# Performance work log

Measured on AMD Instinct MI355X. Metric: run time of the kernel, lower is better.

Reference implementation:

```python
import jax, jax.numpy as jnp
import numpy as np

DX = 0.1
DY = 0.1
W_B = 1000.0
W_PARALLEL = 1000.0
W_DIV = 100.0
EPS = 1e-10


def setup_inputs() -> dict:
    key = jax.random.key(0)
    k1, k2 = jax.random.split(key)
    outputs = jax.random.normal(k1, (2, 3, 256, 256, 64), dtype=jnp.float32)
    targets = jax.random.normal(k2, (2, 4, 256, 256, 64), dtype=jnp.float32)
    return {"outputs": outputs, "targets": targets}


def _corners(f):
    # 8 shifted views f[..., i:, j:, k:] (with 0 -> [0:-1], 1 -> [1:]) on dims 2,3,4
    s0, s1 = slice(0, -1), slice(1, None)
    return {(i, j, k): f[:, :, (s1 if i else s0), (s1 if j else s0), (s1 if k else s0)]
            for i in (0, 1) for j in (0, 1) for k in (0, 1)}


def _forward(outputs, targets):
    bx_p, by_p, bz_p = outputs[:, 0:1], outputs[:, 1:2], outputs[:, 2:3]
    bx_t, by_t, bz_t = targets[:, 0:1], targets[:, 1:2], targets[:, 2:3]

    loss_b = (jnp.mean((bx_p**2 + by_p**2 - bx_t**2 - by_t**2) ** 2 / (bx_t**2 + by_t**2 + EPS))
              + jnp.mean((bz_p - bz_t) ** 4 / (bz_t**2 + EPS)))
    loss_parallel = jnp.mean((bx_p * by_t - by_p * bx_t) ** 2
                             / (bx_t**2 + by_t**2 + bz_t**2 + EPS))

    bx = _corners(bx_p)
    by = _corners(by_p)
    bz = _corners(bz_p)
    z = _corners(targets[:, 3:4])

    num = (0.25 * (bx[1, 0, 0] + bx[1, 1, 0] + bx[1, 0, 1] + bx[1, 1, 1]) * DY * 0.5 * (z[1, 0, 1] - z[1, 0, 0] + z[1, 1, 1] - z[1, 1, 0])
           - 0.25 * (bx[0, 0, 0] + bx[0, 1, 0] + bx[0, 0, 1] + bx[0, 1, 1]) * DY * 0.5 * (z[0, 0, 1] - z[0, 0, 0] + z[0, 1, 1] - z[0, 1, 0])
           + 0.25 * (by[0, 1, 0] + by[1, 1, 0] + by[0, 1, 1] + by[1, 1, 1]) * DX * 0.5 * (z[0, 1, 1] - z[0, 1, 0] + z[1, 1, 1] - z[1, 1, 0])
           - 0.25 * (by[0, 0, 0] + by[1, 0, 0] + by[0, 0, 1] + by[1, 0, 1]) * DX * 0.5 * (z[0, 0, 1] - z[0, 0, 0] + z[1, 0, 1] - z[1, 0, 0])
           + 0.25 * (bz[0, 0, 1] + bz[0, 1, 1] + bz[1, 0, 1] + bz[1, 1, 1]) * DX * DY
           - 0.25 * (bz[0, 0, 0] + bz[0, 1, 0] + bz[1, 0, 0] + bz[1, 1, 0]) * DX * DY
           + (bx[0, 0, 1] + bx[1, 0, 1] + bx[1, 1, 1]) * DY * (z[0, 0, 1] - z[1, 0, 1]) / 6
           + (bx[0, 1, 1] + bx[1, 1, 1] + bx[1, 0, 1]) * DY * (z[0, 1, 1] - z[1, 1, 1]) / 6
           + (by[1, 0, 1] + by[1, 1, 1] + by[0, 1, 1]) * DX * (z[1, 0, 1] - z[1, 1, 1]) / 6
           + (by[0, 0, 1] + by[0, 1, 1] + by[1, 1, 1]) * DX * (z[0, 0, 1] - z[0, 1, 1]) / 6
           - (bx[0, 0, 0] + bx[1, 0, 0] + bx[1, 1, 0]) * DY * (z[0, 0, 0] - z[1, 0, 0]) / 6
           - (bx[0, 1, 0] + bx[1, 1, 0] + bx[1, 0, 0]) * DY * (z[0, 1, 0] - z[1, 1, 0]) / 6
           - (by[1, 0, 0] + by[1, 1, 0] + by[0, 1, 0]) * DX * (z[1, 0, 0] - z[1, 1, 0]) / 6
           - (by[0, 0, 0] + by[0, 1, 0] + by[1, 1, 0]) * DX * (z[0, 0, 0] - z[0, 1, 0]) / 6)

    bx_c = sum(bx[c] for c in sorted(bx)) * 0.125
    by_c = sum(by[c] for c in sorted(by)) * 0.125
    bz_c = sum(bz[c] for c in sorted(bz)) * 0.125
    den = bx_c**2 + by_c**2 + bz_c**2 + EPS

    loss_div = jnp.mean(num**2 / den) / DX**2 / DY**2

    return (W_B * loss_b + W_PARALLEL * loss_parallel, W_DIV * loss_div)


def reference(outputs, targets):
    return _forward(outputs, targets)
```

## Files before the change

kernel.cpp:

```cpp
#include <hip/hip_runtime.h>
#include <stdint.h>

constexpr int B = 2, X = 256, Y = 256, Z = 64;
constexpr int CO = X * Y * Z;
constexpr int YZ = Y * Z;
constexpr long long N_PTS   = (long long)B * X * Y * Z;
constexpr long long M_CELLS = (long long)B * (X-1) * (Y-1) * (Z-1);

constexpr int RPB = 16;
constexpr int TPB = 256;
constexpr int WPB = TPB / 64;
constexpr int BLOCKS = B * (Y / RPB) * X;

constexpr int SSTRIDE = 1152;

#define EPSc 1e-10f
#define SIXTH (1.0f / 6.0f)
#define RCPF(v) __builtin_amdgcn_rcpf(v)

typedef float fvec4 __attribute__((ext_vector_type(4)));

#define F4C(v, c) (((c) == 0) ? (v).x : ((c) == 1) ? (v).y : ((c) == 2) ? (v).z : (v).w)

typedef const __attribute__((address_space(1))) uint32_t* gptr_t;
typedef __attribute__((address_space(3))) uint32_t* lptr_t;

__global__ __launch_bounds__(TPB, 4) void loss_main(const float* __restrict__ outs,
                                                    const float* __restrict__ tgts,
                                                    double* __restrict__ partial) {
    __shared__ float sm[8 * SSTRIDE];

    const int lane = threadIdx.x & 63;
    const int wv   = threadIdx.x >> 6;
    const int blk  = blockIdx.x;

    const int b  = blk >> 12;
    const int r  = blk & 4095;
    const int sy = r >> 8;
    const int x  = r & 255;
    const int y0 = sy * RPB;
    const int xc1 = (x + 1 < X) ? (x + 1) : (X - 1);
    const bool xvalid = (x < X - 1);

    const float* ob = outs + (size_t)b * 3 * CO;
    const float* tb = tgts + (size_t)b * 4 * CO;

    const int row_l = wv * 4 + (lane >> 4);
    const int zi    = (lane & 15) << 2;
    const int y_own = y0 + row_l;
    const bool yvalid = (y_own < Y - 1);

    const float* tb0 = tb + (size_t)x * YZ + (size_t)y_own * Z + zi;
    const fvec4 tbx = __builtin_nontemporal_load((const fvec4*)(tb0 + 0 * CO));
    const fvec4 tby = __builtin_nontemporal_load((const fvec4*)(tb0 + 1 * CO));
    const fvec4 tbz = __builtin_nontemporal_load((const fvec4*)(tb0 + 2 * CO));

    const int y16 = (y0 + 16 < Y) ? (y0 + 16) : (Y - 1);
    #pragma unroll
    for (int j = 0; j < 2; ++j) {
        const int s   = wv * 2 + j;
        const int col = s >> 2;
        const int ch  = s & 3;
        const int xs  = col ? xc1 : x;
        const float* gbase = (ch < 3 ? ob + (size_t)ch * CO : tb + (size_t)3 * CO)
                           + (size_t)xs * YZ;
        const float* gsrc  = gbase + (size_t)y0 * Z;
        float* ldst = sm + s * SSTRIDE;
        #pragma unroll
        for (int k = 0; k < 4; ++k) {
            __builtin_amdgcn_global_load_lds((gptr_t)(gsrc + k * 256 + lane * 4),
                                             (lptr_t)(ldst + k * 256 + lane * 4),
                                             16, 0, 0);
        }
        const float* gsrc16 = gbase + (size_t)y16 * Z;
        __builtin_amdgcn_global_load_lds((gptr_t)(gsrc16 + lane),
                                         (lptr_t)(ldst + 16 * 64 + lane),
                                         4, 0, 0);
    }
    __syncthreads();

    #define SMF4(col, ch, row) (*(const fvec4*)(sm + ((col) * 4 + (ch)) * SSTRIDE + (row) * 64 + zi))

    const fvec4 obx   = SMF4(0, 0, row_l);
    const fvec4 oby   = SMF4(0, 1, row_l);
    const fvec4 obz   = SMF4(0, 2, row_l);
    const fvec4 tzc   = SMF4(0, 3, row_l);
    const fvec4 obx1  = SMF4(1, 0, row_l);
    const fvec4 oby1  = SMF4(1, 1, row_l);
    const fvec4 obz1  = SMF4(1, 2, row_l);
    const fvec4 tzc1  = SMF4(1, 3, row_l);
    const fvec4 obxy  = SMF4(0, 0, row_l + 1);
    const fvec4 obyy  = SMF4(0, 1, row_l + 1);
    const fvec4 obzy  = SMF4(0, 2, row_l + 1);
    const fvec4 tzcy  = SMF4(0, 3, row_l + 1);
    const fvec4 obxy1 = SMF4(1, 0, row_l + 1);
    const fvec4 obyy1 = SMF4(1, 1, row_l + 1);
    const fvec4 obzy1 = SMF4(1, 2, row_l + 1);
    const fvec4 tzcy1 = SMF4(1, 3, row_l + 1);

    double s_pt = 0.0;
    double s_dv = 0.0;

    {
        float pt4 = 0.0f;
        #pragma unroll
        for (int c = 0; c < 4; ++c) {
            const float bxp = F4C(obx, c), byp = F4C(oby, c), bzp = F4C(obz, c);
            const float bxt = F4C(tbx, c), byt = F4C(tby, c), bzt = F4C(tbz, c);
            const float bxt2 = bxt * bxt, byt2 = byt * byt, bzt2 = bzt * bzt;
            const float dxy = bxt2 + byt2;
            const float t1 = bxp * bxp + byp * byp - dxy;
            const float e1 = t1 * t1 * RCPF(dxy + EPSc);
            const float dd = bzp - bzt;
            const float dd2 = dd * dd;
            const float e2 = dd2 * dd2 * RCPF(bzt2 + EPSc);
            const float cr = bxp * byt - byp * bxt;
            const float e3 = cr * cr * RCPF(dxy + bzt2 + EPSc);
            pt4 += e1 + e2 + e3;
        }
        s_pt += (double)pt4;
    }

    if (xvalid) {
        float sxp[5], sxm[5], syp[5], sym[5];
        float zxp[5], zxm[5], zyp[5], zym[5];
        float Sx[5], Sy[5], Sz[5], G2[5];

        #pragma unroll
        for (int t = 0; t < 4; ++t) {
            const float bx00 = F4C(obx, t),   bx10 = F4C(obx1, t);
            const float bx01 = F4C(obxy, t),  bx11 = F4C(obxy1, t);
            const float by00 = F4C(oby, t),   by10 = F4C(oby1, t);
            const float by01 = F4C(obyy, t),  by11 = F4C(obyy1, t);
            const float bz00 = F4C(obz, t),   bz10 = F4C(obz1, t);
            const float bz01 = F4C(obzy, t),  bz11 = F4C(obzy1, t);
            const float zc00 = F4C(tzc, t),   zc10 = F4C(tzc1, t);
            const float zc01 = F4C(tzcy, t),  zc11 = F4C(tzcy1, t);

            sxp[t] = bx10 + bx11;   sxm[t] = bx00 + bx01;
            syp[t] = by01 + by11;   sym[t] = by00 + by10;
            zxp[t] = zc10 + zc11;   zxm[t] = zc00 + zc01;
            zyp[t] = zc01 + zc11;   zym[t] = zc00 + zc10;
            Sx[t] = sxp[t] + sxm[t];
            Sy[t] = syp[t] + sym[t];
            Sz[t] = (bz00 + bz01) + (bz10 + bz11);
            G2[t] = 0.025f * Sz[t]
                  + SIXTH * ((bx00 + sxp[t]) * (zc00 - zc10)
                           + (bx01 + sxp[t]) * (zc01 - zc11)
                           + (by10 + syp[t]) * (zc10 - zc11)
                           + (by00 + syp[t]) * (zc00 - zc01));
        }
        sxp[4] = __shfl_down(sxp[0], 1);
        sxm[4] = __shfl_down(sxm[0], 1);
        syp[4] = __shfl_down(syp[0], 1);
        sym[4] = __shfl_down(sym[0], 1);
        zxp[4] = __shfl_down(zxp[0], 1);
        zxm[4] = __shfl_down(zxm[0], 1);
        zyp[4] = __shfl_down(zyp[0], 1);
        zym[4] = __shfl_down(zym[0], 1);
        Sz[4]  = __shfl_down(Sz[0],  1);
        G2[4]  = __shfl_down(G2[0],  1);
        Sx[4] = sxp[4] + sxm[4];
        Sy[4] = syp[4] + sym[4];

        float dv4 = 0.0f;
        #pragma unroll
        for (int c = 0; c < 4; ++c) {
            const float fx = (sxp[c] + sxp[c+1]) * (zxp[c+1] - zxp[c])
                           - (sxm[c] + sxm[c+1]) * (zxm[c+1] - zxm[c])
                           + (syp[c] + syp[c+1]) * (zyp[c+1] - zyp[c])
                           - (sym[c] + sym[c+1]) * (zym[c+1] - zym[c]);
            const float num2 = 0.125f * fx + (G2[c+1] - G2[c]);
            const float SxS = Sx[c] + Sx[c+1];
            const float SyS = Sy[c] + Sy[c+1];
            const float SzS = Sz[c] + Sz[c+1];
            const float q = SxS * SxS + SyS * SyS + SzS * SzS;
            const float den = 0.015625f * q + EPSc;
            const float v = num2 * num2 * RCPF(den);
            const bool ok = yvalid && ((zi + c) < Z - 1);
            dv4 += ok ? v : 0.0f;
        }
        s_dv += (double)dv4;
    }

    for (int off = 32; off > 0; off >>= 1) {
        s_pt += __shfl_down(s_pt, off);
        s_dv += __shfl_down(s_dv, off);
    }

    __shared__ double lds_pt[WPB];
    __shared__ double lds_dv[WPB];
    if (lane == 0) { lds_pt[wv] = s_pt; lds_dv[wv] = s_dv; }
    __syncthreads();
    if (threadIdx.x == 0) {
        double p = 0.0, d = 0.0;
        #pragma unroll
        for (int w = 0; w < WPB; ++w) { p += lds_pt[w]; d += lds_dv[w]; }
        partial[2 * blockIdx.x]     = p;
        partial[2 * blockIdx.x + 1] = d;
    }
}

__global__ __launch_bounds__(256) void loss_finalize(const double* __restrict__ partial,
                                                     float* __restrict__ out) {
    double s0 = 0.0, s1 = 0.0;
    for (int i = threadIdx.x; i < BLOCKS; i += 256) {
        s0 += partial[2 * i];
        s1 += partial[2 * i + 1];
    }
    const int lane = threadIdx.x & 63;
    const int wave = threadIdx.x >> 6;
    for (int off = 32; off > 0; off >>= 1) {
        s0 += __shfl_down(s0, off);
        s1 += __shfl_down(s1, off);
    }
    __shared__ double l0[4], l1[4];
    if (lane == 0) { l0[wave] = s0; l1[wave] = s1; }
    __syncthreads();
    if (threadIdx.x == 0) {
        double p = 0.0, d = 0.0;
        #pragma unroll
        for (int w = 0; w < 4; ++w) { p += l0[w]; d += l1[w]; }
        const double out0 = 1000.0 * (p / (double)N_PTS);
        const double out1 = 10000.0 * (d / (double)M_CELLS);
        out[0] = (float)out0;
        out[1] = (float)out1;
    }
}

extern "C" void kernel_launch(void* const* d_in, const int* in_sizes, int n_in,
                              void* d_out, int out_size, void* d_ws, size_t ws_size,
                              hipStream_t stream) {
    const float* outs = (const float*)d_in[0];
    const float* tgts = (const float*)d_in[1];
    float* out = (float*)d_out;
    double* partial = (double*)d_ws;

    loss_main<<<BLOCKS, TPB, 0, stream>>>(outs, tgts, partial);
    loss_finalize<<<1, 256, 0, stream>>>(partial, out);
}
```

Before: 254.6 us.

## March each block along x with a triple-buffered LDS plane pipeline

Each block now handles a strip of 16 consecutive x-planes instead of one. It keeps three rotating LDS buffers so every staged x-plane is reused as both the current and the previous column, and it prefetches the next plane with global_load_lds while computing the current one. This roughly halves the redundant loads of the x+1 neighbour plane and overlaps loads with compute. The cost is fewer blocks (512), lower occupancy (launch bounds 2) and a barrier per step, which may leave latency exposed.

```diff
diff --git a/kernel.cpp b/kernel.cpp
--- a/kernel.cpp
+++ b/kernel.cpp
@@ -8,11 +8,13 @@
 constexpr long long M_CELLS = (long long)B * (X-1) * (Y-1) * (Z-1);
 
 constexpr int RPB = 16;
+constexpr int XS  = 16;
 constexpr int TPB = 256;
 constexpr int WPB = TPB / 64;
-constexpr int BLOCKS = B * (Y / RPB) * X;
-
-constexpr int SSTRIDE = 1152;
+constexpr int BLOCKS = B * (Y / RPB) * (X / XS);
+
+constexpr int CHS  = 1152;
+constexpr int BUFS = 4 * CHS;
 
 #define EPSc 1e-10f
 #define SIXTH (1.0f / 6.0f)
@@ -25,22 +27,21 @@
 typedef const __attribute__((address_space(1))) uint32_t* gptr_t;
 typedef __attribute__((address_space(3))) uint32_t* lptr_t;
 
-__global__ __launch_bounds__(TPB, 4) void loss_main(const float* __restrict__ outs,
+__global__ __launch_bounds__(TPB, 2) void loss_main(const float* __restrict__ outs,
                                                     const float* __restrict__ tgts,
                                                     double* __restrict__ partial) {
-    __shared__ float sm[8 * SSTRIDE];
+    __shared__ __align__(16) float sm[3 * BUFS];
 
     const int lane = threadIdx.x & 63;
     const int wv   = threadIdx.x >> 6;
     const int blk  = blockIdx.x;
 
-    const int b  = blk >> 12;
-    const int r  = blk & 4095;
-    const int sy = r >> 8;
-    const int x  = r & 255;
+    const int b  = blk >> 8;
+    const int r  = blk & 255;
+    const int sy = r >> 4;
+    const int xc = r & 15;
     const int y0 = sy * RPB;
-    const int xc1 = (x + 1 < X) ? (x + 1) : (X - 1);
-    const bool xvalid = (x < X - 1);
+    const int x0 = xc * XS;
 
     const float* ob = outs + (size_t)b * 3 * CO;
     const float* tb = tgts + (size_t)b * 4 * CO;
@@ -49,138 +50,166 @@
     const int zi    = (lane & 15) << 2;
     const int y_own = y0 + row_l;
     const bool yvalid = (y_own < Y - 1);
-
-    const float* tb0 = tb + (size_t)x * YZ + (size_t)y_own * Z + zi;
-    const fvec4 tbx = __builtin_nontemporal_load((const fvec4*)(tb0 + 0 * CO));
-    const fvec4 tby = __builtin_nontemporal_load((const fvec4*)(tb0 + 1 * CO));
-    const fvec4 tbz = __builtin_nontemporal_load((const fvec4*)(tb0 + 2 * CO));
-
     const int y16 = (y0 + 16 < Y) ? (y0 + 16) : (Y - 1);
-    #pragma unroll
-    for (int j = 0; j < 2; ++j) {
-        const int s   = wv * 2 + j;
-        const int col = s >> 2;
-        const int ch  = s & 3;
-        const int xs  = col ? xc1 : x;
-        const float* gbase = (ch < 3 ? ob + (size_t)ch * CO : tb + (size_t)3 * CO)
-                           + (size_t)xs * YZ;
-        const float* gsrc  = gbase + (size_t)y0 * Z;
-        float* ldst = sm + s * SSTRIDE;
+
+    const float* chbase = (wv < 3) ? (ob + (size_t)wv * CO) : (tb + (size_t)3 * CO);
+
+    const float* tnt = tb + (size_t)y_own * Z + zi;
+
+    auto stage = [&](int xs, float* buf) {
+        const float* gbase = chbase + (size_t)xs * YZ;
+        float* ldst = buf + wv * CHS;
+        const float* gsrc = gbase + (size_t)y0 * Z;
         #pragma unroll
         for (int k = 0; k < 4; ++k) {
             __builtin_amdgcn_global_load_lds((gptr_t)(gsrc + k * 256 + lane * 4),
                                              (lptr_t)(ldst + k * 256 + lane * 4),
                                              16, 0, 0);
         }
-        const float* gsrc16 = gbase + (size_t)y16 * Z;
-        __builtin_amdgcn_global_load_lds((gptr_t)(gsrc16 + lane),
+        __builtin_amdgcn_global_load_lds((gptr_t)(gbase + (size_t)y16 * Z + lane),
                                          (lptr_t)(ldst + 16 * 64 + lane),
                                          4, 0, 0);
+    };
+
+    float* prv = sm + 2 * BUFS;
+    float* cur = sm;
+    float* nxt = sm + BUFS;
+
+    stage(x0, cur);
+    fvec4 tc0, tc1, tc2;
+    fvec4 tn0 = {0,0,0,0}, tn1 = {0,0,0,0}, tn2 = {0,0,0,0};
+    {
+        const float* p = tnt + (size_t)x0 * YZ;
+        tc0 = __builtin_nontemporal_load((const fvec4*)(p + 0 * CO));
+        tc1 = __builtin_nontemporal_load((const fvec4*)(p + 1 * CO));
+        tc2 = __builtin_nontemporal_load((const fvec4*)(p + 2 * CO));
     }
     __syncthreads();
 
-    #define SMF4(col, ch, row) (*(const fvec4*)(sm + ((col) * 4 + (ch)) * SSTRIDE + (row) * 64 + zi))
-
-    const fvec4 obx   = SMF4(0, 0, row_l);
-    const fvec4 oby   = SMF4(0, 1, row_l);
-    const fvec4 obz   = SMF4(0, 2, row_l);
-    const fvec4 tzc   = SMF4(0, 3, row_l);
-    const fvec4 obx1  = SMF4(1, 0, row_l);
-    const fvec4 oby1  = SMF4(1, 1, row_l);
-    const fvec4 obz1  = SMF4(1, 2, row_l);
-    const fvec4 tzc1  = SMF4(1, 3, row_l);
-    const fvec4 obxy  = SMF4(0, 0, row_l + 1);
-    const fvec4 obyy  = SMF4(0, 1, row_l + 1);
-    const fvec4 obzy  = SMF4(0, 2, row_l + 1);
-    const fvec4 tzcy  = SMF4(0, 3, row_l + 1);
-    const fvec4 obxy1 = SMF4(1, 0, row_l + 1);
-    const fvec4 obyy1 = SMF4(1, 1, row_l + 1);
-    const fvec4 obzy1 = SMF4(1, 2, row_l + 1);
-    const fvec4 tzcy1 = SMF4(1, 3, row_l + 1);
-
-    double s_pt = 0.0;
-    double s_dv = 0.0;
-
-    {
-        float pt4 = 0.0f;
-        #pragma unroll
-        for (int c = 0; c < 4; ++c) {
-            const float bxp = F4C(obx, c), byp = F4C(oby, c), bzp = F4C(obz, c);
-            const float bxt = F4C(tbx, c), byt = F4C(tby, c), bzt = F4C(tbz, c);
-            const float bxt2 = bxt * bxt, byt2 = byt * byt, bzt2 = bzt * bzt;
-            const float dxy = bxt2 + byt2;
-            const float t1 = bxp * bxp + byp * byp - dxy;
-            const float e1 = t1 * t1 * RCPF(dxy + EPSc);
-            const float dd = bzp - bzt;
-            const float dd2 = dd * dd;
-            const float e2 = dd2 * dd2 * RCPF(bzt2 + EPSc);
-            const float cr = bxp * byt - byp * bxt;
-            const float e3 = cr * cr * RCPF(dxy + bzt2 + EPSc);
-            pt4 += e1 + e2 + e3;
-        }
-        s_pt += (double)pt4;
-    }
-
-    if (xvalid) {
-        float sxp[5], sxm[5], syp[5], sym[5];
-        float zxp[5], zxm[5], zyp[5], zym[5];
-        float Sx[5], Sy[5], Sz[5], G2[5];
-
-        #pragma unroll
-        for (int t = 0; t < 4; ++t) {
-            const float bx00 = F4C(obx, t),   bx10 = F4C(obx1, t);
-            const float bx01 = F4C(obxy, t),  bx11 = F4C(obxy1, t);
-            const float by00 = F4C(oby, t),   by10 = F4C(oby1, t);
-            const float by01 = F4C(obyy, t),  by11 = F4C(obyy1, t);
-            const float bz00 = F4C(obz, t),   bz10 = F4C(obz1, t);
-            const float bz01 = F4C(obzy, t),  bz11 = F4C(obzy1, t);
-            const float zc00 = F4C(tzc, t),   zc10 = F4C(tzc1, t);
-            const float zc01 = F4C(tzcy, t),  zc11 = F4C(tzcy1, t);
-
-            sxp[t] = bx10 + bx11;   sxm[t] = bx00 + bx01;
-            syp[t] = by01 + by11;   sym[t] = by00 + by10;
-            zxp[t] = zc10 + zc11;   zxm[t] = zc00 + zc01;
-            zyp[t] = zc01 + zc11;   zym[t] = zc00 + zc10;
-            Sx[t] = sxp[t] + sxm[t];
-            Sy[t] = syp[t] + sym[t];
-            Sz[t] = (bz00 + bz01) + (bz10 + bz11);
-            G2[t] = 0.025f * Sz[t]
-                  + SIXTH * ((bx00 + sxp[t]) * (zc00 - zc10)
-                           + (bx01 + sxp[t]) * (zc01 - zc11)
-                           + (by10 + syp[t]) * (zc10 - zc11)
-                           + (by00 + syp[t]) * (zc00 - zc01));
-        }
-        sxp[4] = __shfl_down(sxp[0], 1);
-        sxm[4] = __shfl_down(sxm[0], 1);
-        syp[4] = __shfl_down(syp[0], 1);
-        sym[4] = __shfl_down(sym[0], 1);
-        zxp[4] = __shfl_down(zxp[0], 1);
-        zxm[4] = __shfl_down(zxm[0], 1);
-        zyp[4] = __shfl_down(zyp[0], 1);
-        zym[4] = __shfl_down(zym[0], 1);
-        Sz[4]  = __shfl_down(Sz[0],  1);
-        G2[4]  = __shfl_down(G2[0],  1);
-        Sx[4] = sxp[4] + sxm[4];
-        Sy[4] = syp[4] + sym[4];
-
-        float dv4 = 0.0f;
-        #pragma unroll
-        for (int c = 0; c < 4; ++c) {
-            const float fx = (sxp[c] + sxp[c+1]) * (zxp[c+1] - zxp[c])
-                           - (sxm[c] + sxm[c+1]) * (zxm[c+1] - zxm[c])
-                           + (syp[c] + syp[c+1]) * (zyp[c+1] - zyp[c])
-                           - (sym[c] + sym[c+1]) * (zym[c+1] - zym[c]);
-            const float num2 = 0.125f * fx + (G2[c+1] - G2[c]);
-            const float SxS = Sx[c] + Sx[c+1];
-            const float SyS = Sy[c] + Sy[c+1];
-            const float SzS = Sz[c] + Sz[c+1];
-            const float q = SxS * SxS + SyS * SyS + SzS * SzS;
-            const float den = 0.015625f * q + EPSc;
-            const float v = num2 * num2 * RCPF(den);
-            const bool ok = yvalid && ((zi + c) < Z - 1);
-            dv4 += ok ? v : 0.0f;
-        }
-        s_dv += (double)dv4;
+    double s_pt = 0.0, s_dv = 0.0;
+
+    #define SMF4(base, ch, row) (*(const fvec4*)((base) + (ch) * CHS + (row) * 64 + zi))
+
+    #pragma unroll 1
+    for (int i = 0; i <= XS; ++i) {
+        if (i < XS) {
+            int xs1 = x0 + i + 1;
+            if (xs1 > X - 1) xs1 = X - 1;
+            stage(xs1, nxt);
+            if (i + 1 < XS) {
+                const float* p = tnt + (size_t)(x0 + i + 1) * YZ;
+                tn0 = __builtin_nontemporal_load((const fvec4*)(p + 0 * CO));
+                tn1 = __builtin_nontemporal_load((const fvec4*)(p + 1 * CO));
+                tn2 = __builtin_nontemporal_load((const fvec4*)(p + 2 * CO));
+            }
+        }
+
+        if (i < XS) {
+            const fvec4 obx = SMF4(cur, 0, row_l);
+            const fvec4 oby = SMF4(cur, 1, row_l);
+            const fvec4 obz = SMF4(cur, 2, row_l);
+            float pt4 = 0.0f;
+            #pragma unroll
+            for (int c = 0; c < 4; ++c) {
+                const float bxp = F4C(obx, c), byp = F4C(oby, c), bzp = F4C(obz, c);
+                const float bxt = F4C(tc0, c), byt = F4C(tc1, c), bzt = F4C(tc2, c);
+                const float bxt2 = bxt * bxt, byt2 = byt * byt, bzt2 = bzt * bzt;
+                const float dxy = bxt2 + byt2;
+                const float t1 = bxp * bxp + byp * byp - dxy;
+                const float e1 = t1 * t1 * RCPF(dxy + EPSc);
+                const float dd = bzp - bzt;
+                const float dd2 = dd * dd;
+                const float e2 = dd2 * dd2 * RCPF(bzt2 + EPSc);
+                const float cr = bxp * byt - byp * bxt;
+                const float e3 = cr * cr * RCPF(dxy + bzt2 + EPSc);
+                pt4 += e1 + e2 + e3;
+            }
+            s_pt += (double)pt4;
+        }
+
+        if (i >= 1 && (x0 + i - 1) < X - 1) {
+            const fvec4 obx   = SMF4(prv, 0, row_l);
+            const fvec4 oby   = SMF4(prv, 1, row_l);
+            const fvec4 obz   = SMF4(prv, 2, row_l);
+            const fvec4 tzc   = SMF4(prv, 3, row_l);
+            const fvec4 obx1  = SMF4(cur, 0, row_l);
+            const fvec4 oby1  = SMF4(cur, 1, row_l);
+            const fvec4 obz1  = SMF4(cur, 2, row_l);
+            const fvec4 tzc1  = SMF4(cur, 3, row_l);
+            const fvec4 obxy  = SMF4(prv, 0, row_l + 1);
+            const fvec4 obyy  = SMF4(prv, 1, row_l + 1);
+            const fvec4 obzy  = SMF4(prv, 2, row_l + 1);
+            const fvec4 tzcy  = SMF4(prv, 3, row_l + 1);
+            const fvec4 obxy1 = SMF4(cur, 0, row_l + 1);
+            const fvec4 obyy1 = SMF4(cur, 1, row_l + 1);
+            const fvec4 obzy1 = SMF4(cur, 2, row_l + 1);
+            const fvec4 tzcy1 = SMF4(cur, 3, row_l + 1);
+
+            float sxp[5], sxm[5], syp[5], sym[5];
+            float zxp[5], zxm[5], zyp[5], zym[5];
+            float Sx[5], Sy[5], Sz[5], G2[5];
+
+            #pragma unroll
+            for (int t = 0; t < 4; ++t) {
+                const float bx00 = F4C(obx, t),   bx10 = F4C(obx1, t);
+                const float bx01 = F4C(obxy, t),  bx11 = F4C(obxy1, t);
+                const float by00 = F4C(oby, t),   by10 = F4C(oby1, t);
+                const float by01 = F4C(obyy, t),  by11 = F4C(obyy1, t);
+                const float bz00 = F4C(obz, t),   bz10 = F4C(obz1, t);
+                const float bz01 = F4C(obzy, t),  bz11 = F4C(obzy1, t);
+                const float zc00 = F4C(tzc, t),   zc10 = F4C(tzc1, t);
+                const float zc01 = F4C(tzcy, t),  zc11 = F4C(tzcy1, t);
+
+                sxp[t] = bx10 + bx11;   sxm[t] = bx00 + bx01;
+                syp[t] = by01 + by11;   sym[t] = by00 + by10;
+                zxp[t] = zc10 + zc11;   zxm[t] = zc00 + zc01;
+                zyp[t] = zc01 + zc11;   zym[t] = zc00 + zc10;
+                Sx[t] = sxp[t] + sxm[t];
+                Sy[t] = syp[t] + sym[t];
+                Sz[t] = (bz00 + bz01) + (bz10 + bz11);
+                G2[t] = 0.025f * Sz[t]
+                      + SIXTH * ((bx00 + sxp[t]) * (zc00 - zc10)
+                               + (bx01 + sxp[t]) * (zc01 - zc11)
+                               + (by10 + syp[t]) * (zc10 - zc11)
+                               + (by00 + syp[t]) * (zc00 - zc01));
+            }
+            sxp[4] = __shfl_down(sxp[0], 1);
+            sxm[4] = __shfl_down(sxm[0], 1);
+            syp[4] = __shfl_down(syp[0], 1);
+            sym[4] = __shfl_down(sym[0], 1);
+            zxp[4] = __shfl_down(zxp[0], 1);
+            zxm[4] = __shfl_down(zxm[0], 1);
+            zyp[4] = __shfl_down(zyp[0], 1);
+            zym[4] = __shfl_down(zym[0], 1);
+            Sz[4]  = __shfl_down(Sz[0],  1);
+            G2[4]  = __shfl_down(G2[0],  1);
+            Sx[4] = sxp[4] + sxm[4];
+            Sy[4] = syp[4] + sym[4];
+
+            float dv4 = 0.0f;
+            #pragma unroll
+            for (int c = 0; c < 4; ++c) {
+                const float fx = (sxp[c] + sxp[c+1]) * (zxp[c+1] - zxp[c])
+                               - (sxm[c] + sxm[c+1]) * (zxm[c+1] - zxm[c])
+                               + (syp[c] + syp[c+1]) * (zyp[c+1] - zyp[c])
+                               - (sym[c] + sym[c+1]) * (zym[c+1] - zym[c]);
+                const float num2 = 0.125f * fx + (G2[c+1] - G2[c]);
+                const float SxS = Sx[c] + Sx[c+1];
+                const float SyS = Sy[c] + Sy[c+1];
+                const float SzS = Sz[c] + Sz[c+1];
+                const float q = SxS * SxS + SyS * SyS + SzS * SzS;
+                const float den = 0.015625f * q + EPSc;
+                const float v = num2 * num2 * RCPF(den);
+                const bool ok = yvalid && ((zi + c) < Z - 1);
+                dv4 += ok ? v : 0.0f;
+            }
+            s_dv += (double)dv4;
+        }
+
+        if (i < XS) __syncthreads();
+
+        float* tmp = prv; prv = cur; cur = nxt; nxt = tmp;
+        tc0 = tn0; tc1 = tn1; tc2 = tn2;
     }
 
     for (int off = 32; off > 0; off >>= 1) {
```

Result: faster. 247.6 us (-2.7%).

## Replace LDS staging with direct global loads and swizzle block order

Applied to the files above, without the earlier changes.

Drops the global_load_lds staging into shared memory and the barrier that followed it. Each thread now loads its four corner neighbours straight from global memory with vector loads and relies on L2/L1 to serve the overlapping rows and columns. The block index is also remapped in strides of BLOCKS/8, apparently to spread neighbouring blocks across XCDs or improve cache locality. This removes LDS traffic and the sync, but each thread now issues four times as many global loads, and cache reuse is not guaranteed.

```diff
diff --git a/kernel.cpp b/kernel.cpp
--- a/kernel.cpp
+++ b/kernel.cpp
@@ -12,8 +12,6 @@
 constexpr int WPB = TPB / 64;
 constexpr int BLOCKS = B * (Y / RPB) * X;
 
-constexpr int SSTRIDE = 1152;
-
 #define EPSc 1e-10f
 #define SIXTH (1.0f / 6.0f)
 #define RCPF(v) __builtin_amdgcn_rcpf(v)
@@ -21,96 +19,72 @@
 typedef float fvec4 __attribute__((ext_vector_type(4)));
 
 #define F4C(v, c) (((c) == 0) ? (v).x : ((c) == 1) ? (v).y : ((c) == 2) ? (v).z : (v).w)
-
-typedef const __attribute__((address_space(1))) uint32_t* gptr_t;
-typedef __attribute__((address_space(3))) uint32_t* lptr_t;
+#define LD4(p)  (*(const fvec4*)(p))
+#define LDNT(p) __builtin_nontemporal_load((const fvec4*)(p))
 
 __global__ __launch_bounds__(TPB, 4) void loss_main(const float* __restrict__ outs,
                                                     const float* __restrict__ tgts,
                                                     double* __restrict__ partial) {
-    __shared__ float sm[8 * SSTRIDE];
-
     const int lane = threadIdx.x & 63;
     const int wv   = threadIdx.x >> 6;
-    const int blk  = blockIdx.x;
+
+    const int bid = (int)blockIdx.x;
+    const int blk = (bid & 7) * (BLOCKS / 8) + (bid >> 3);
 
     const int b  = blk >> 12;
     const int r  = blk & 4095;
     const int sy = r >> 8;
     const int x  = r & 255;
-    const int y0 = sy * RPB;
-    const int xc1 = (x + 1 < X) ? (x + 1) : (X - 1);
+
+    const int row_l = wv * 4 + (lane >> 4);
+    const int zi    = (lane & 15) << 2;
+    const int y     = sy * RPB + row_l;
+
+    const int xp = (x < X - 1) ? (x + 1) : x;
+    const int yp = (y < Y - 1) ? (y + 1) : y;
     const bool xvalid = (x < X - 1);
+    const bool yvalid = (y < Y - 1);
 
     const float* ob = outs + (size_t)b * 3 * CO;
     const float* tb = tgts + (size_t)b * 4 * CO;
 
-    const int row_l = wv * 4 + (lane >> 4);
-    const int zi    = (lane & 15) << 2;
-    const int y_own = y0 + row_l;
-    const bool yvalid = (y_own < Y - 1);
-
-    const float* tb0 = tb + (size_t)x * YZ + (size_t)y_own * Z + zi;
-    const fvec4 tbx = __builtin_nontemporal_load((const fvec4*)(tb0 + 0 * CO));
-    const fvec4 tby = __builtin_nontemporal_load((const fvec4*)(tb0 + 1 * CO));
-    const fvec4 tbz = __builtin_nontemporal_load((const fvec4*)(tb0 + 2 * CO));
-
-    const int y16 = (y0 + 16 < Y) ? (y0 + 16) : (Y - 1);
-    #pragma unroll
-    for (int j = 0; j < 2; ++j) {
-        const int s   = wv * 2 + j;
-        const int col = s >> 2;
-        const int ch  = s & 3;
-        const int xs  = col ? xc1 : x;
-        const float* gbase = (ch < 3 ? ob + (size_t)ch * CO : tb + (size_t)3 * CO)
-                           + (size_t)xs * YZ;
-        const float* gsrc  = gbase + (size_t)y0 * Z;
-        float* ldst = sm + s * SSTRIDE;
-        #pragma unroll
-        for (int k = 0; k < 4; ++k) {
-            __builtin_amdgcn_global_load_lds((gptr_t)(gsrc + k * 256 + lane * 4),
-                                             (lptr_t)(ldst + k * 256 + lane * 4),
-                                             16, 0, 0);
-        }
-        const float* gsrc16 = gbase + (size_t)y16 * Z;
-        __builtin_amdgcn_global_load_lds((gptr_t)(gsrc16 + lane),
-                                         (lptr_t)(ldst + 16 * 64 + lane),
-                                         4, 0, 0);
-    }
-    __syncthreads();
-
-    #define SMF4(col, ch, row) (*(const fvec4*)(sm + ((col) * 4 + (ch)) * SSTRIDE + (row) * 64 + zi))
-
-    const fvec4 obx   = SMF4(0, 0, row_l);
-    const fvec4 oby   = SMF4(0, 1, row_l);
-    const fvec4 obz   = SMF4(0, 2, row_l);
-    const fvec4 tzc   = SMF4(0, 3, row_l);
-    const fvec4 obx1  = SMF4(1, 0, row_l);
-    const fvec4 oby1  = SMF4(1, 1, row_l);
-    const fvec4 obz1  = SMF4(1, 2, row_l);
-    const fvec4 tzc1  = SMF4(1, 3, row_l);
-    const fvec4 obxy  = SMF4(0, 0, row_l + 1);
-    const fvec4 obyy  = SMF4(0, 1, row_l + 1);
-    const fvec4 obzy  = SMF4(0, 2, row_l + 1);
-    const fvec4 tzcy  = SMF4(0, 3, row_l + 1);
-    const fvec4 obxy1 = SMF4(1, 0, row_l + 1);
-    const fvec4 obyy1 = SMF4(1, 1, row_l + 1);
-    const fvec4 obzy1 = SMF4(1, 2, row_l + 1);
-    const fvec4 tzcy1 = SMF4(1, 3, row_l + 1);
-
-    double s_pt = 0.0;
-    double s_dv = 0.0;
+    const size_t o00 = (size_t)x  * YZ + (size_t)y  * Z + zi;
+    const size_t o01 = (size_t)x  * YZ + (size_t)yp * Z + zi;
+    const size_t o10 = (size_t)xp * YZ + (size_t)y  * Z + zi;
+    const size_t o11 = (size_t)xp * YZ + (size_t)yp * Z + zi;
+
+    const fvec4 bx00v = LD4(ob + 0 * CO + o00);
+    const fvec4 by00v = LD4(ob + 1 * CO + o00);
+    const fvec4 bz00v = LD4(ob + 2 * CO + o00);
+    const fvec4 zc00v = LD4(tb + 3 * CO + o00);
+    const fvec4 bx01v = LD4(ob + 0 * CO + o01);
+    const fvec4 by01v = LD4(ob + 1 * CO + o01);
+    const fvec4 bz01v = LD4(ob + 2 * CO + o01);
+    const fvec4 zc01v = LD4(tb + 3 * CO + o01);
+    const fvec4 bx10v = LD4(ob + 0 * CO + o10);
+    const fvec4 by10v = LD4(ob + 1 * CO + o10);
+    const fvec4 bz10v = LD4(ob + 2 * CO + o10);
+    const fvec4 zc10v = LD4(tb + 3 * CO + o10);
+    const fvec4 bx11v = LD4(ob + 0 * CO + o11);
+    const fvec4 by11v = LD4(ob + 1 * CO + o11);
+    const fvec4 bz11v = LD4(ob + 2 * CO + o11);
+    const fvec4 zc11v = LD4(tb + 3 * CO + o11);
+    const fvec4 t0 = LDNT(tb + 0 * CO + o00);
+    const fvec4 t1 = LDNT(tb + 1 * CO + o00);
+    const fvec4 t2 = LDNT(tb + 2 * CO + o00);
+
+    double s_pt = 0.0, s_dv = 0.0;
 
     {
         float pt4 = 0.0f;
         #pragma unroll
         for (int c = 0; c < 4; ++c) {
-            const float bxp = F4C(obx, c), byp = F4C(oby, c), bzp = F4C(obz, c);
-            const float bxt = F4C(tbx, c), byt = F4C(tby, c), bzt = F4C(tbz, c);
+            const float bxp = F4C(bx00v, c), byp = F4C(by00v, c), bzp = F4C(bz00v, c);
+            const float bxt = F4C(t0, c), byt = F4C(t1, c), bzt = F4C(t2, c);
             const float bxt2 = bxt * bxt, byt2 = byt * byt, bzt2 = bzt * bzt;
             const float dxy = bxt2 + byt2;
-            const float t1 = bxp * bxp + byp * byp - dxy;
-            const float e1 = t1 * t1 * RCPF(dxy + EPSc);
+            const float tq = bxp * bxp + byp * byp - dxy;
+            const float e1 = tq * tq * RCPF(dxy + EPSc);
             const float dd = bzp - bzt;
             const float dd2 = dd * dd;
             const float e2 = dd2 * dd2 * RCPF(bzt2 + EPSc);
@@ -128,14 +102,14 @@
 
         #pragma unroll
         for (int t = 0; t < 4; ++t) {
-            const float bx00 = F4C(obx, t),   bx10 = F4C(obx1, t);
-            const float bx01 = F4C(obxy, t),  bx11 = F4C(obxy1, t);
-            const float by00 = F4C(oby, t),   by10 = F4C(oby1, t);
-            const float by01 = F4C(obyy, t),  by11 = F4C(obyy1, t);
-            const float bz00 = F4C(obz, t),   bz10 = F4C(obz1, t);
-            const float bz01 = F4C(obzy, t),  bz11 = F4C(obzy1, t);
-            const float zc00 = F4C(tzc, t),   zc10 = F4C(tzc1, t);
-            const float zc01 = F4C(tzcy, t),  zc11 = F4C(tzcy1, t);
+            const float bx00 = F4C(bx00v, t), bx10 = F4C(bx10v, t);
+            const float bx01 = F4C(bx01v, t), bx11 = F4C(bx11v, t);
+            const float by00 = F4C(by00v, t), by10 = F4C(by10v, t);
+            const float by01 = F4C(by01v, t), by11 = F4C(by11v, t);
+            const float bz00 = F4C(bz00v, t), bz10 = F4C(bz10v, t);
+            const float bz01 = F4C(bz01v, t), bz11 = F4C(bz11v, t);
+            const float zc00 = F4C(zc00v, t), zc10 = F4C(zc10v, t);
+            const float zc01 = F4C(zc01v, t), zc11 = F4C(zc11v, t);
 
             sxp[t] = bx10 + bx11;   sxm[t] = bx00 + bx01;
             syp[t] = by01 + by11;   sym[t] = by00 + by10;
@@ -196,8 +170,8 @@
         double p = 0.0, d = 0.0;
         #pragma unroll
         for (int w = 0; w < WPB; ++w) { p += lds_pt[w]; d += lds_dv[w]; }
-        partial[2 * blockIdx.x]     = p;
-        partial[2 * blockIdx.x + 1] = d;
+        partial[2 * blk]     = p;
+        partial[2 * blk + 1] = d;
     }
 }
 
```

Result: slower. 269.1 us (+5.7%).
